# Performance work log

Hardware: AMD Instinct MI355X
Metric: run time of the kernel (lower is better)

## Reference

```python
import jax, jax.numpy as jnp
import numpy as np

B, H, K, D = 4096, 3, 32768, 128


def setup_inputs() -> dict:
    key = jax.random.key(0)
    k_in, k_emb = jax.random.split(key)
    inputs = jax.random.normal(k_in, (B, 1, D), dtype=jnp.float32)
    # xavier-uniform-ish init with per-head decay 0.5**h (gain 6.0), as in the module
    ks = jax.random.split(k_emb, H)
    tables = []
    for h in range(H):
        gain = 6.0 * (0.5 ** h)
        bound = gain * np.sqrt(6.0 / (K + D))
        tables.append(jax.random.uniform(ks[h], (K, D), jnp.float32, -bound, bound))
    emb = jnp.stack(tables, axis=0)  # [H, K, D]
    return {"inputs": inputs, "emb": emb}


def reference(inputs, emb):
    # Eval-mode HRQ forward: per-head negative squared-L2 distances to the
    # codebook on the running residual, hard argmax assignment, summed codes.
    x = inputs[:, 0, :]                      # [B, D]
    n_heads = emb.shape[0]
    resid = x
    quantized = jnp.zeros_like(x)
    codes = []
    for h in range(n_heads):
        W = emb[h]                            # [K, D]
        # -(||r||^2 + ||w||^2 - 2 r.w)  -> argmax == nearest code
        dists = -(jnp.sum(resid * resid, axis=1, keepdims=True)
                  + jnp.sum(W * W, axis=1)
                  - 2.0 * resid @ W.T)        # [B, K]
        c = jnp.argmax(dists, axis=-1)        # [B]
        q = jnp.take(W, c, axis=0)            # onehot(c) @ W == gather
        resid = resid - q
        quantized = quantized + q
        codes.append(c)
    loss = jnp.zeros(x.shape[0], dtype=inputs.dtype)
    return loss, quantized.reshape(inputs.shape), jnp.stack(codes, axis=1)
```

## Files before the change

### kernel.cpp

```cpp
#include <hip/hip_runtime.h>
#include <math.h>

#define NB 4096
#define NH 3
#define NK 32768
#define ND 128
#define KA 256
#define KB 256
#define RB 64
#define CS 16
#define CPB (NK / CS)
#define CI 256
#define NCI (CPB / CI)

typedef _Float16 half8_t __attribute__((ext_vector_type(8)));
typedef _Float16 half2_t __attribute__((ext_vector_type(2)));
typedef float f32x4 __attribute__((ext_vector_type(4)));
typedef __attribute__((address_space(1))) const unsigned int gu32_t;
typedef __attribute__((address_space(3))) unsigned int lu32_t;

__global__ __launch_bounds__(64) void init_kernel(const float* __restrict__ inp,
                                                  float* __restrict__ resid,
                                                  float* __restrict__ rr,
                                                  float* __restrict__ out,
                                                  _Float16* __restrict__ Aext) {
  int row = blockIdx.x;
  int lane = threadIdx.x;
  const float2* ip = (const float2*)(inp + row * ND);
  float2 v = ip[lane];
  ((float2*)(resid + row * ND))[lane] = v;
  ((float2*)(out + NB + row * ND))[lane] = make_float2(0.f, 0.f);
  if (lane == 0) out[row] = 0.f;
  _Float16 h0 = (_Float16)v.x, h1 = (_Float16)v.y;
  _Float16 l0 = (_Float16)(v.x - (float)h0), l1 = (_Float16)(v.y - (float)h1);
  half2_t h = {h0, h1}, l = {l0, l1};
  _Float16* base = Aext + (size_t)row * KA;
  *(half2_t*)(base + 2 * lane) = h;
  *(half2_t*)(base + 128 + 2 * lane) = l;
  float s = v.x * v.x + v.y * v.y;
  #pragma unroll
  for (int m = 32; m; m >>= 1) s += __shfl_xor(s, m, 64);
  if (lane == 0) rr[row] = s;
}

__global__ __launch_bounds__(256) void norms_kernel(const float* __restrict__ emb,
                                                    float* __restrict__ norms) {
  int row = blockIdx.x * 4 + (threadIdx.x >> 6);
  int lane = threadIdx.x & 63;
  const float2* wp = (const float2*)(emb + (size_t)row * ND);
  float2 v = wp[lane];
  float s = v.x * v.x + v.y * v.y;
  #pragma unroll
  for (int m = 32; m; m >>= 1) s += __shfl_xor(s, m, 64);
  if (lane == 0) norms[row] = s;
}

__global__ __launch_bounds__(256) void split_w_all_kernel(const float* __restrict__ emb,
                                                          _Float16* __restrict__ Bext) {
  const int head = blockIdx.x >> 11;
  const int cg = blockIdx.x & 2047;
  const int n_lo = threadIdx.x & 15;
  const int c = threadIdx.x >> 4;
  const int n = cg * 16 + n_lo;

  const float4* wp = (const float4*)(emb + (size_t)head * NK * ND + (size_t)n * ND + c * 8);
  float4 v0 = wp[0], v1 = wp[1];
  float xv[8] = {v0.x, v0.y, v0.z, v0.w, v1.x, v1.y, v1.z, v1.w};
  half8_t h, l;
  #pragma unroll
  for (int j = 0; j < 8; ++j) {
    _Float16 hh = (_Float16)xv[j];
    h[j] = hh;
    l[j] = (_Float16)(xv[j] - (float)hh);
  }
  const int ks0 = c >> 2;
  const int klo = c & 3;
  _Float16* base = Bext + (size_t)head * NK * KB + (size_t)(cg >> 2) * 16384 +
                   (cg & 3) * 512 + klo * 128 + n_lo * 8;
  *(half8_t*)(base + ks0 * 2048) = h;
  *(half8_t*)(base + (4 + ks0) * 2048) = l;
}

__global__ __launch_bounds__(256, 2) void score_mfma_kernel(
    const _Float16* __restrict__ Aext, const _Float16* __restrict__ Bext,
    const float* __restrict__ rr, const float* __restrict__ normh,
    float* __restrict__ partial_s, int* __restrict__ partial_i) {
  __shared__ __align__(16) _Float16 Ash[RB * KA];

  const int bid = blockIdx.x;
  const int cs = bid & 15;
  const int rowb = bid >> 4;
  const int rowBase = rowb * RB;
  const int colBase0 = cs * CPB;

  const int tid = threadIdx.x;
  const int lane = tid & 63;
  const int wn = tid >> 6;
  const int l15 = lane & 15;
  const int q = lane >> 4;

  {
    const int mrow = lane >> 3;
    const int cg = (lane & 7) ^ (mrow & 7);
    #pragma unroll
    for (int i = 0; i < 8; ++i) {
      int wc = wn * 8 + i;
      int p = wc >> 3;
      int m0 = (wc & 7) * 8;
      const _Float16* gA = Aext + (size_t)(rowBase + m0 + mrow) * KA + p * 64 + cg * 8;
      __builtin_amdgcn_global_load_lds((gu32_t*)gA, (lu32_t*)&Ash[(p * 64 + m0) * 64], 16, 0, 0);
    }
  }

  int aaddr[2][4];
  #pragma unroll
  for (int par = 0; par < 2; ++par)
    #pragma unroll
    for (int mt = 0; mt < 4; ++mt) {
      int m = mt * 16 + l15;
      int slot = (par * 4 + q) ^ (m & 7);
      aaddr[par][mt] = (m * 8 + slot) * 16;
    }

  float rv[16];
  #pragma unroll
  for (int mt = 0; mt < 4; ++mt)
    #pragma unroll
    for (int reg = 0; reg < 4; ++reg)
      rv[mt * 4 + reg] = rr[rowBase + mt * 16 + q * 4 + reg];

  float bs[16];
  int bi[16];
  #pragma unroll
  for (int t = 0; t < 16; ++t) { bs[t] = -INFINITY; bi[t] = 0x7fffffff; }

  __syncthreads();

  #pragma unroll 1
  for (int ci = NCI - 1; ci >= 0; --ci) {
    const int ncol = colBase0 + ci * CI + wn * 64;
    const unsigned int boff = (unsigned int)(ncol >> 6) * 16384u + (unsigned int)lane * 8u;

    f32x4 acc[4][4];
    #pragma unroll
    for (int i = 0; i < 4; ++i)
      #pragma unroll
      for (int j = 0; j < 4; ++j) acc[i][j] = (f32x4){0.f, 0.f, 0.f, 0.f};

    #pragma unroll 2
    for (int kc = 0; kc < 4; ++kc) {
      half8_t bh[4], bl[4];
      #pragma unroll
      for (int tn = 0; tn < 4; ++tn) {
        bh[tn] = *(const half8_t*)(Bext + boff + (unsigned int)(kc * 2048 + tn * 512));
        bl[tn] = *(const half8_t*)(Bext + boff + (unsigned int)((4 + kc) * 2048 + tn * 512));
      }
      const int par = kc & 1, p = kc >> 1;
      half8_t afh[4], afl[4];
      #pragma unroll
      for (int mt = 0; mt < 4; ++mt) {
        afh[mt] = *(const half8_t*)((const char*)Ash + aaddr[par][mt] + p * 8192);
        afl[mt] = *(const half8_t*)((const char*)Ash + aaddr[par][mt] + 16384 + p * 8192);
      }
      #pragma unroll
      for (int mt = 0; mt < 4; ++mt)
        #pragma unroll
        for (int tn = 0; tn < 4; ++tn)
          acc[mt][tn] = __builtin_amdgcn_mfma_f32_16x16x32_f16(afh[mt], bh[tn], acc[mt][tn], 0, 0, 0);
      #pragma unroll
      for (int mt = 0; mt < 4; ++mt)
        #pragma unroll
        for (int tn = 0; tn < 4; ++tn)
          acc[mt][tn] = __builtin_amdgcn_mfma_f32_16x16x32_f16(afl[mt], bh[tn], acc[mt][tn], 0, 0, 0);
      #pragma unroll
      for (int mt = 0; mt < 4; ++mt)
        #pragma unroll
        for (int tn = 0; tn < 4; ++tn)
          acc[mt][tn] = __builtin_amdgcn_mfma_f32_16x16x32_f16(afh[mt], bl[tn], acc[mt][tn], 0, 0, 0);
    }

    #pragma unroll
    for (int tn = 3; tn >= 0; --tn) {
      float nw = normh[ncol + tn * 16 + l15];
      int cidx = ncol + tn * 16 + l15;
      #pragma unroll
      for (int mt = 0; mt < 4; ++mt) {
        #pragma unroll
        for (int reg = 0; reg < 4; ++reg) {
          const int s = mt * 4 + reg;
          float t1 = rv[s] + nw;
          float v = fmaf(2.0f, acc[mt][tn][reg], -t1);
          if (v >= bs[s]) { bs[s] = v; bi[s] = cidx; }
        }
      }
    }
  }

  __syncthreads();
  float* red_s = (float*)Ash;
  int* red_i = (int*)Ash + RB * 4;
  #pragma unroll
  for (int t = 0; t < 16; ++t) {
    float s = bs[t];
    int ii = bi[t];
    #pragma unroll
    for (int mask = 1; mask <= 8; mask <<= 1) {
      float os = __shfl_xor(s, mask, 64);
      int oi = __shfl_xor(ii, mask, 64);
      if (os > s || (os == s && oi < ii)) { s = os; ii = oi; }
    }
    if (l15 == 0) {
      int rloc = (t >> 2) * 16 + q * 4 + (t & 3);
      red_s[rloc * 4 + wn] = s;
      red_i[rloc * 4 + wn] = ii;
    }
  }
  __syncthreads();
  if (tid < RB) {
    float s0 = red_s[tid * 4];
    int i0 = red_i[tid * 4];
    #pragma unroll
    for (int x = 1; x < 4; ++x) {
      float sx = red_s[tid * 4 + x];
      int ix = red_i[tid * 4 + x];
      if (sx > s0 || (sx == s0 && ix < i0)) { s0 = sx; i0 = ix; }
    }
    partial_s[(size_t)(rowBase + tid) * CS + cs] = s0;
    partial_i[(size_t)(rowBase + tid) * CS + cs] = i0;
  }
}

__global__ __launch_bounds__(64) void reduce_update_kernel(const float* __restrict__ embh,
                                                           float* __restrict__ resid,
                                                           float* __restrict__ rr,
                                                           const float* __restrict__ ps,
                                                           const int* __restrict__ pi,
                                                           float* __restrict__ out,
                                                           _Float16* __restrict__ Aext, int h) {
  int row = blockIdx.x;
  int lane = threadIdx.x;
  float bs = -INFINITY;
  int bi = 0x7fffffff;
  if (lane < CS) {
    bs = ps[(size_t)row * CS + lane];
    bi = pi[(size_t)row * CS + lane];
  }
  #pragma unroll
  for (int m = 8; m; m >>= 1) {
    float os = __shfl_xor(bs, m, 64);
    int oi = __shfl_xor(bi, m, 64);
    if (os > bs || (os == bs && oi < bi)) { bs = os; bi = oi; }
  }
  int c = __shfl(bi, 0, 64);
  if (lane == 0) out[NB + NB * ND + row * NH + h] = (float)c;

  const float* wv = embh + (size_t)c * ND;
  float q0 = wv[lane], q1 = wv[lane + 64];
  float r0 = resid[row * ND + lane] - q0;
  float r1 = resid[row * ND + lane + 64] - q1;
  resid[row * ND + lane] = r0;
  resid[row * ND + lane + 64] = r1;
  out[NB + row * ND + lane] += q0;
  out[NB + row * ND + lane + 64] += q1;

  _Float16 h0 = (_Float16)r0, l0 = (_Float16)(r0 - (float)h0);
  _Float16 h1 = (_Float16)r1, l1 = (_Float16)(r1 - (float)h1);
  _Float16* ab = Aext + (size_t)row * KA;
  ab[lane] = h0;       ab[lane + 64] = h1;
  ab[128 + lane] = l0; ab[128 + lane + 64] = l1;

  float s = r0 * r0 + r1 * r1;
  #pragma unroll
  for (int m = 32; m; m >>= 1) s += __shfl_xor(s, m, 64);
  if (lane == 0) rr[row] = s;
}

extern "C" void kernel_launch(void* const* d_in, const int* in_sizes, int n_in,
                              void* d_out, int out_size, void* d_ws, size_t ws_size,
                              hipStream_t stream) {
  const float* inp = (const float*)d_in[0];
  const float* emb = (const float*)d_in[1];
  float* out = (float*)d_out;

  float* resid = (float*)d_ws;
  float* rr = resid + NB * ND;
  float* norms = rr + NB;
  float* ps = norms + NH * NK;
  int* pi = (int*)(ps + (size_t)NB * CS);
  _Float16* Aext = (_Float16*)(pi + (size_t)NB * CS);
  _Float16* Bext = Aext + (size_t)NB * KA;

  hipLaunchKernelGGL(init_kernel, dim3(NB), dim3(64), 0, stream, inp, resid, rr, out, Aext);
  hipLaunchKernelGGL(norms_kernel, dim3(NH * NK / 4), dim3(256), 0, stream, emb, norms);
  hipLaunchKernelGGL(split_w_all_kernel, dim3(NH * NK / 16), dim3(256), 0, stream, emb, Bext);
  for (int h = 0; h < NH; ++h) {
    hipLaunchKernelGGL(score_mfma_kernel, dim3((NB / RB) * CS), dim3(256), 0, stream,
                       Aext, Bext + (size_t)h * NK * KB, rr, norms + (size_t)h * NK, ps, pi);
    hipLaunchKernelGGL(reduce_update_kernel, dim3(NB), dim3(64), 0, stream,
                       emb + (size_t)h * NK * ND, resid, rr, ps, pi, out, Aext, h);
  }
}
```

Baseline: 427.8 us.

## Software-pipeline B loads and deferred argmax fold, double column splits

Restructures the score loop so B fragments for the next k-chunk (and next column tile) are prefetched while the current MFMAs run, and the argmax fold of the previous tile is deferred to overlap with the next tile's loads. Row norms move to shared memory to cut register use. The column split count grows from 16 to 32, doubling the grid to improve occupancy and tail balance, at the cost of more partial results to reduce and more redundant A staging per block.

```diff
diff --git a/kernel.cpp b/kernel.cpp
--- a/kernel.cpp
+++ b/kernel.cpp
@@ -8,7 +8,7 @@
 #define KA 256
 #define KB 256
 #define RB 64
-#define CS 16
+#define CS 32
 #define CPB (NK / CS)
 #define CI 256
 #define NCI (CPB / CI)
@@ -86,10 +86,11 @@
     const float* __restrict__ rr, const float* __restrict__ normh,
     float* __restrict__ partial_s, int* __restrict__ partial_i) {
   __shared__ __align__(16) _Float16 Ash[RB * KA];
+  __shared__ __align__(16) float rrsh[RB];
 
   const int bid = blockIdx.x;
-  const int cs = bid & 15;
-  const int rowb = bid >> 4;
+  const int cs = bid & (CS - 1);
+  const int rowb = bid / CS;
   const int rowBase = rowb * RB;
   const int colBase0 = cs * CPB;
 
@@ -111,23 +112,15 @@
       __builtin_amdgcn_global_load_lds((gu32_t*)gA, (lu32_t*)&Ash[(p * 64 + m0) * 64], 16, 0, 0);
     }
   }
-
-  int aaddr[2][4];
-  #pragma unroll
-  for (int par = 0; par < 2; ++par)
-    #pragma unroll
-    for (int mt = 0; mt < 4; ++mt) {
-      int m = mt * 16 + l15;
-      int slot = (par * 4 + q) ^ (m & 7);
-      aaddr[par][mt] = (m * 8 + slot) * 16;
-    }
-
-  float rv[16];
-  #pragma unroll
-  for (int mt = 0; mt < 4; ++mt)
-    #pragma unroll
-    for (int reg = 0; reg < 4; ++reg)
-      rv[mt * 4 + reg] = rr[rowBase + mt * 16 + q * 4 + reg];
+  if (tid < RB) rrsh[tid] = rr[rowBase + tid];
+
+  int aaddr0[4];
+  #pragma unroll
+  for (int mt = 0; mt < 4; ++mt) {
+    int m = mt * 16 + l15;
+    int slot = q ^ (m & 7);
+    aaddr0[mt] = (m * 8 + slot) * 16;
+  }
 
   float bs[16];
   int bi[16];
@@ -136,65 +129,98 @@
 
   __syncthreads();
 
+  const f32x4 Z = {0.f, 0.f, 0.f, 0.f};
+  f32x4 acc[4][4];
+  half8_t bh[4], bl[4];
+  float pnw[4];
+  int pncol = 0;
+
+#define A_HI(MT_, KC_) (*(const half8_t*)((const char*)Ash + \
+    ((aaddr0[MT_] ^ (((KC_) & 1) << 6)) + ((KC_) >> 1) * 8192)))
+#define A_LO(MT_, KC_) (*(const half8_t*)((const char*)Ash + \
+    ((aaddr0[MT_] ^ (((KC_) & 1) << 6)) + ((KC_) >> 1) * 8192 + 16384)))
+
+#define LOADB(BOFF_, KC_) do { \
+    _Pragma("unroll") \
+    for (int tn = 0; tn < 4; ++tn) { \
+      bh[tn] = *(const half8_t*)(Bext + (BOFF_) + (unsigned)((KC_) * 2048 + tn * 512)); \
+      bl[tn] = *(const half8_t*)(Bext + (BOFF_) + (unsigned)(((KC_) + 4) * 2048 + tn * 512)); \
+    } \
+  } while (0)
+
+#define MFMA_KC(KC_, ZEROC_) do { \
+    half8_t afh[4], afl[4]; \
+    _Pragma("unroll") \
+    for (int mt = 0; mt < 4; ++mt) { afh[mt] = A_HI(mt, KC_); afl[mt] = A_LO(mt, KC_); } \
+    _Pragma("unroll") \
+    for (int mt = 0; mt < 4; ++mt) \
+      _Pragma("unroll") \
+      for (int tn = 0; tn < 4; ++tn) \
+        acc[mt][tn] = __builtin_amdgcn_mfma_f32_16x16x32_f16(afh[mt], bh[tn], \
+            (ZEROC_) ? Z : acc[mt][tn], 0, 0, 0); \
+    _Pragma("unroll") \
+    for (int mt = 0; mt < 4; ++mt) \
+      _Pragma("unroll") \
+      for (int tn = 0; tn < 4; ++tn) \
+        acc[mt][tn] = __builtin_amdgcn_mfma_f32_16x16x32_f16(afl[mt], bh[tn], acc[mt][tn], 0, 0, 0); \
+    _Pragma("unroll") \
+    for (int mt = 0; mt < 4; ++mt) \
+      _Pragma("unroll") \
+      for (int tn = 0; tn < 4; ++tn) \
+        acc[mt][tn] = __builtin_amdgcn_mfma_f32_16x16x32_f16(afh[mt], bl[tn], acc[mt][tn], 0, 0, 0); \
+  } while (0)
+
+#define FOLD() do { \
+    f32x4 rvv[4]; \
+    _Pragma("unroll") \
+    for (int mt = 0; mt < 4; ++mt) rvv[mt] = *(const f32x4*)&rrsh[mt * 16 + q * 4]; \
+    _Pragma("unroll") \
+    for (int tn = 3; tn >= 0; --tn) { \
+      float nwv = pnw[tn]; \
+      int cidx = pncol + tn * 16 + l15; \
+      _Pragma("unroll") \
+      for (int mt = 0; mt < 4; ++mt) { \
+        _Pragma("unroll") \
+        for (int reg = 0; reg < 4; ++reg) { \
+          const int s = mt * 4 + reg; \
+          float t1 = rvv[mt][reg] + nwv;                \
+          float v = fmaf(2.0f, acc[mt][tn][reg], -t1);  \
+          if (v >= bs[s]) { bs[s] = v; bi[s] = cidx; } \
+        } \
+      } \
+    } \
+  } while (0)
+
+  {
+    const int ncol0 = colBase0 + (NCI - 1) * CI + wn * 64;
+    const unsigned boff0 = (unsigned)(ncol0 >> 6) * 16384u + (unsigned)lane * 8u;
+    LOADB(boff0, 0);
+  }
+
   #pragma unroll 1
   for (int ci = NCI - 1; ci >= 0; --ci) {
-    const int ncol = colBase0 + ci * CI + wn * 64;
-    const unsigned int boff = (unsigned int)(ncol >> 6) * 16384u + (unsigned int)lane * 8u;
-
-    f32x4 acc[4][4];
-    #pragma unroll
-    for (int i = 0; i < 4; ++i)
-      #pragma unroll
-      for (int j = 0; j < 4; ++j) acc[i][j] = (f32x4){0.f, 0.f, 0.f, 0.f};
-
-    #pragma unroll 2
-    for (int kc = 0; kc < 4; ++kc) {
-      half8_t bh[4], bl[4];
-      #pragma unroll
-      for (int tn = 0; tn < 4; ++tn) {
-        bh[tn] = *(const half8_t*)(Bext + boff + (unsigned int)(kc * 2048 + tn * 512));
-        bl[tn] = *(const half8_t*)(Bext + boff + (unsigned int)((4 + kc) * 2048 + tn * 512));
-      }
-      const int par = kc & 1, p = kc >> 1;
-      half8_t afh[4], afl[4];
-      #pragma unroll
-      for (int mt = 0; mt < 4; ++mt) {
-        afh[mt] = *(const half8_t*)((const char*)Ash + aaddr[par][mt] + p * 8192);
-        afl[mt] = *(const half8_t*)((const char*)Ash + aaddr[par][mt] + 16384 + p * 8192);
-      }
-      #pragma unroll
-      for (int mt = 0; mt < 4; ++mt)
-        #pragma unroll
-        for (int tn = 0; tn < 4; ++tn)
-          acc[mt][tn] = __builtin_amdgcn_mfma_f32_16x16x32_f16(afh[mt], bh[tn], acc[mt][tn], 0, 0, 0);
-      #pragma unroll
-      for (int mt = 0; mt < 4; ++mt)
-        #pragma unroll
-        for (int tn = 0; tn < 4; ++tn)
-          acc[mt][tn] = __builtin_amdgcn_mfma_f32_16x16x32_f16(afl[mt], bh[tn], acc[mt][tn], 0, 0, 0);
-      #pragma unroll
-      for (int mt = 0; mt < 4; ++mt)
-        #pragma unroll
-        for (int tn = 0; tn < 4; ++tn)
-          acc[mt][tn] = __builtin_amdgcn_mfma_f32_16x16x32_f16(afh[mt], bl[tn], acc[mt][tn], 0, 0, 0);
-    }
-
-    #pragma unroll
-    for (int tn = 3; tn >= 0; --tn) {
-      float nw = normh[ncol + tn * 16 + l15];
-      int cidx = ncol + tn * 16 + l15;
-      #pragma unroll
-      for (int mt = 0; mt < 4; ++mt) {
-        #pragma unroll
-        for (int reg = 0; reg < 4; ++reg) {
-          const int s = mt * 4 + reg;
-          float t1 = rv[s] + nw;
-          float v = fmaf(2.0f, acc[mt][tn][reg], -t1);
-          if (v >= bs[s]) { bs[s] = v; bi[s] = cidx; }
-        }
-      }
-    }
-  }
+    const int ncol_c = colBase0 + ci * CI + wn * 64;
+    const unsigned boff_c = (unsigned)(ncol_c >> 6) * 16384u + (unsigned)lane * 8u;
+    const int ci_n = (ci > 0) ? ci - 1 : 0;
+    const unsigned boff_n =
+        (unsigned)((colBase0 + ci_n * CI + wn * 64) >> 6) * 16384u + (unsigned)lane * 8u;
+
+    float nw[4];
+    #pragma unroll
+    for (int tn = 0; tn < 4; ++tn) nw[tn] = normh[ncol_c + tn * 16 + l15];
+
+    if (ci != NCI - 1) FOLD();
+
+    MFMA_KC(0, 1); LOADB(boff_c, 1);
+    MFMA_KC(1, 0); LOADB(boff_c, 2);
+    MFMA_KC(2, 0); LOADB(boff_c, 3);
+    MFMA_KC(3, 0); LOADB(boff_n, 0);
+
+    #pragma unroll
+    for (int tn = 0; tn < 4; ++tn) pnw[tn] = nw[tn];
+    pncol = ncol_c;
+  }
+  FOLD();
 
   __syncthreads();
   float* red_s = (float*)Ash;
@@ -228,6 +254,11 @@
     partial_s[(size_t)(rowBase + tid) * CS + cs] = s0;
     partial_i[(size_t)(rowBase + tid) * CS + cs] = i0;
   }
+#undef A_HI
+#undef A_LO
+#undef LOADB
+#undef MFMA_KC
+#undef FOLD
 }
 
 __global__ __launch_bounds__(64) void reduce_update_kernel(const float* __restrict__ embh,
@@ -246,7 +277,7 @@
     bi = pi[(size_t)row * CS + lane];
   }
   #pragma unroll
-  for (int m = 8; m; m >>= 1) {
+  for (int m = CS >> 1; m; m >>= 1) {
     float os = __shfl_xor(bs, m, 64);
     int oi = __shfl_xor(bi, m, 64);
     if (os > bs || (os == bs && oi < bi)) { bs = os; bi = oi; }
```

After: 991.8 us. +131.8%, slower.
